# Optimization experiments

Measured on AMD Instinct MI355X. Metric: run time of the kernel, lower is better.

The kernel has to match this reference:

```python
import jax, jax.numpy as jnp
import numpy as np

N = 100_000      # nodes
E = 1_600_000    # edges
F_IN = 512       # input node features
H = 128          # hidden (num_hidden)
C = 64           # num_classes


def setup_inputs() -> dict:
    key = jax.random.key(0)
    ks = jax.random.split(key, 16)
    def lin(k, fi, fo):
        return (jax.random.normal(k, (fi, fo), jnp.float32) / np.sqrt(fi)).astype(jnp.float32)
    inp = {
        'x': jax.random.normal(ks[0], (N, F_IN), jnp.float32),
        'edge_index': jax.random.randint(ks[1], (2, E), 0, N, jnp.int32),
        'W0': lin(ks[2], F_IN, H), 'b0': jnp.zeros((H,), jnp.float32),
        'W1': lin(ks[3], H, H),    'b1': jnp.zeros((H,), jnp.float32),
        'W2': lin(ks[4], H, H),    'b2': jnp.zeros((H,), jnp.float32),
        'fc1_w': lin(ks[5], H, H), 'fc1_b': jnp.zeros((H,), jnp.float32),
        'fc2_w': lin(ks[6], H, H), 'fc2_b': jnp.zeros((H,), jnp.float32),
        'fc3_w': lin(ks[7], H, C), 'fc3_b': jnp.zeros((C,), jnp.float32),
    }
    return inp


def _gcn_norm(edge_index):
    # PyG GCNConv: add self-loops, symmetric normalization deg^-1/2 A deg^-1/2
    src = jnp.concatenate([edge_index[0], jnp.arange(N, dtype=edge_index.dtype)])
    dst = jnp.concatenate([edge_index[1], jnp.arange(N, dtype=edge_index.dtype)])
    deg = jax.ops.segment_sum(jnp.ones_like(dst, jnp.float32), dst, num_segments=N)
    dinv = jnp.where(deg > 0, jax.lax.rsqrt(deg), 0.0)
    norm = dinv[src] * dinv[dst]  # [E+N]
    return src, dst, norm


def _gcn_conv(x, W, b, src, dst, norm):
    h = x @ W + b                      # [N, H] transform first (fewer flops when F_in > H)
    msg = h[src] * norm[:, None]       # gather + scale, [E+N, H]
    return jax.ops.segment_sum(msg, dst, num_segments=N)  # scatter-add


def reference(x, edge_index, W0, b0, W1, b1, W2, b2,
              fc1_w, fc1_b, fc2_w, fc2_b, fc3_w, fc3_b):
    src, dst, norm = _gcn_norm(edge_index)
    y = jax.nn.relu(_gcn_conv(x, W0, b0, src, dst, norm))
    y = jax.nn.relu(_gcn_conv(y, W1, b1, src, dst, norm))
    y = jax.nn.relu(_gcn_conv(y, W2, b2, src, dst, norm))
    y = jax.nn.relu(y @ fc1_w + fc1_b)
    y = jax.nn.relu(y @ fc2_w + fc2_b)
    y = y @ fc3_w + fc3_b
    return jax.nn.log_softmax(y, axis=1)
```

## Files before the change

kernel.cpp:

```cpp
#include <hip/hip_runtime.h>
#include <hip/hip_bf16.h>
#include <cstdint>

typedef __hip_bfloat16 bf16;
typedef __hip_bfloat162 bf162;
typedef __bf16 bf16x8 __attribute__((ext_vector_type(8)));
typedef float f32x4 __attribute__((ext_vector_type(4)));

__global__ void detect_kernel(const unsigned short* __restrict__ xr, int* __restrict__ flag) {
  if (threadIdx.x == 0 && blockIdx.x == 0) {
    int pass = 0;
    for (int i = 0; i < 64; ++i) {
      unsigned short h = xr[2 * i];
      int e = (h >> 7) & 0xFF;
      if (e >= 110 && e <= 140) pass++;
    }
    *flag = (pass >= 32) ? 1 : 0;
  }
}

struct CvtDesc {
  const void* src;
  void* dst;
  int n, fi, fo, mode;
};
struct CvtAll { CvtDesc d[12]; };

__global__ void convert_all_kernel(CvtAll all, const int* __restrict__ flag) {
  CvtDesc dd = all.d[blockIdx.y];
  int isbf = *flag;
  for (int i = blockIdx.x * blockDim.x + threadIdx.x; i < dd.n; i += gridDim.x * blockDim.x) {
    float v = isbf ? __bfloat162float(((const bf16*)dd.src)[i]) : ((const float*)dd.src)[i];
    if (dd.mode) {
      int k = i / dd.fo, nn = i - k * dd.fo;
      ((__bf16*)dd.dst)[(size_t)nn * dd.fi + k] = (__bf16)v;
    } else {
      ((float*)dd.dst)[i] = v;
    }
  }
}


__global__ void count_kernel(const int* __restrict__ dst, int* __restrict__ deg, int E) {
  int i = blockIdx.x * blockDim.x + threadIdx.x;
  if (i < E) atomicAdd(&deg[dst[i]], 1);
}

__global__ void dinv_kernel(const int* __restrict__ deg, float* __restrict__ dinv, int n) {
  int i = blockIdx.x * blockDim.x + threadIdx.x;
  if (i < n) dinv[i] = rsqrtf((float)(deg[i] + 1));
}

__global__ void scan_block_kernel(const int* __restrict__ counts, int* __restrict__ excl,
                                  int* __restrict__ bsum, int n) {
  __shared__ int sd[1024];
  int t = threadIdx.x;
  int i = blockIdx.x * 1024 + t;
  int v = (i < n) ? counts[i] : 0;
  sd[t] = v;
  __syncthreads();
  for (int off = 1; off < 1024; off <<= 1) {
    int x = (t >= off) ? sd[t - off] : 0;
    __syncthreads();
    sd[t] += x;
    __syncthreads();
  }
  if (i < n) excl[i] = sd[t] - v;
  if (t == 1023) bsum[blockIdx.x] = sd[1023];
}

__global__ void scan_sums_kernel(int* __restrict__ bsum, int nb, int* __restrict__ row_ptr, int n) {
  __shared__ int sd[1024];
  int t = threadIdx.x;
  int v = (t < nb) ? bsum[t] : 0;
  sd[t] = v;
  __syncthreads();
  for (int off = 1; off < 1024; off <<= 1) {
    int x = (t >= off) ? sd[t - off] : 0;
    __syncthreads();
    sd[t] += x;
    __syncthreads();
  }
  if (t < nb) bsum[t] = sd[t] - v;
  if (t == 1023) row_ptr[n] = sd[1023];
}

__global__ void scan_add_kernel(int* __restrict__ excl, const int* __restrict__ bsum, int n) {
  int i = blockIdx.x * blockDim.x + threadIdx.x;
  if (i < n) excl[i] += bsum[i >> 10];
}

__global__ void fill_kernel(const int* __restrict__ src, const int* __restrict__ dst,
                            const int* __restrict__ row_ptr, int* __restrict__ cursor,
                            int* __restrict__ col, int E) {
  int i = blockIdx.x * blockDim.x + threadIdx.x;
  if (i < E) {
    int d = dst[i];
    int pos = row_ptr[d] + atomicAdd(&cursor[d], 1);
    col[pos] = src[i];
  }
}

__device__ __forceinline__ void gload_lds16(const void* g, void* l) {
  __builtin_amdgcn_global_load_lds(
      (const __attribute__((address_space(1))) void*)g,
      (__attribute__((address_space(3))) void*)l, 16, 0, 0);
}


template <int K, int ADUAL>
__global__ __launch_bounds__(256) void gemm_mfma_kernel(
    const void* __restrict__ Ain, const __bf16* __restrict__ Bt,
    const float* __restrict__ bias, bf16* __restrict__ C,
    int M, const float* __restrict__ rowscale, int do_relu,
    const int* __restrict__ flag) {
  constexpr int BK = 64;
  constexpr int NT = K / BK;
  __shared__ __align__(16) __bf16 As[2][128 * BK];
  __shared__ __align__(16) __bf16 Bs[2][128 * BK];

  const int abf = ADUAL ? flag[0] : 1;
  int t = threadIdx.x;
  int wave = t >> 6, lane = t & 63;
  int l15 = lane & 15, quad = lane >> 4;
  int wm = wave >> 1, wn = wave & 1;
  int rowbase = blockIdx.x * 128;
  const __bf16* Ab = (const __bf16*)Ain;
  const float* Af = (const float*)Ain;

  int srow = t >> 3;
  int sslot = t & 7;
  int xslot = sslot ^ (srow & 7);

  int sArow[4];
#pragma unroll
  for (int i = 0; i < 4; ++i) {
    int r = rowbase + i * 32 + srow;
    sArow[i] = (r < M) ? r : (M - 1);
  }

  f32x4 acc[4][4];
#pragma unroll
  for (int mt = 0; mt < 4; ++mt)
#pragma unroll
    for (int nt = 0; nt < 4; ++nt) acc[mt][nt] = (f32x4){0.f, 0.f, 0.f, 0.f};

  auto stage = [&](int kt, int buf) {
    int kbase = kt * BK + xslot * 8;
    if (abf) {
#pragma unroll
      for (int i = 0; i < 4; ++i)
        gload_lds16(Ab + (size_t)sArow[i] * K + kbase, &As[buf][t * 8 + i * 2048]);
    } else {
#pragma unroll
      for (int i = 0; i < 4; ++i) {
        const float* p = Af + (size_t)sArow[i] * K + kbase;
        bf16x8 v;
#pragma unroll
        for (int j = 0; j < 8; ++j) v[j] = (__bf16)p[j];
        *(bf16x8*)&As[buf][t * 8 + i * 2048] = v;
      }
    }
#pragma unroll
    for (int i = 0; i < 4; ++i)
      gload_lds16(Bt + (size_t)(i * 32 + srow) * K + kbase, &Bs[buf][t * 8 + i * 2048]);
  };

  auto compute = [&](int buf) {
#pragma unroll
    for (int c = 0; c < 2; ++c) {
      bf16x8 av[4], bv[4];
#pragma unroll
      for (int mt = 0; mt < 4; ++mt) {
        int row = wm * 64 + mt * 16 + l15;
        int slot = (c * 4 + quad) ^ (row & 7);
        av[mt] = *(const bf16x8*)&As[buf][row * BK + slot * 8];
      }
#pragma unroll
      for (int nt = 0; nt < 4; ++nt) {
        int row = wn * 64 + nt * 16 + l15;
        int slot = (c * 4 + quad) ^ (row & 7);
        bv[nt] = *(const bf16x8*)&Bs[buf][row * BK + slot * 8];
      }
#pragma unroll
      for (int mt = 0; mt < 4; ++mt)
#pragma unroll
        for (int nt = 0; nt < 4; ++nt)
          acc[mt][nt] =
              __builtin_amdgcn_mfma_f32_16x16x32_bf16(av[mt], bv[nt], acc[mt][nt], 0, 0, 0);
    }
  };

  stage(0, 0);
  __syncthreads();
#pragma unroll
  for (int kt = 0; kt < NT; ++kt) {
    int cur = kt & 1;
    if (kt + 1 < NT) stage(kt + 1, cur ^ 1);
    compute(cur);
    __syncthreads();
  }

#pragma unroll
  for (int mt = 0; mt < 4; ++mt) {
    int r0 = rowbase + wm * 64 + mt * 16 + quad * 4;
#pragma unroll
    for (int nt = 0; nt < 4; ++nt) {
      int c = wn * 64 + nt * 16 + l15;
      float bs = bias[c];
#pragma unroll
      for (int i = 0; i < 4; ++i) {
        int r = r0 + i;
        if (r < M) {
          float v = acc[mt][nt][i] + bs;
          if (rowscale) v *= rowscale[r];
          if (do_relu) v = fmaxf(v, 0.f);
          C[(size_t)r * 128 + c] = __float2bfloat16(v);
        }
      }
    }
  }
}


__global__ __launch_bounds__(256) void gather_kernel(
    const bf16* __restrict__ g, const int* __restrict__ row_ptr, const int* __restrict__ col,
    const float* __restrict__ dinv, bf16* __restrict__ y, int n) {
  int wave = threadIdx.x >> 6;
  int lane = threadIdx.x & 63;
  int node = blockIdx.x * 4 + wave;
  if (node >= n) return;
  const bf162* gp = (const bf162*)g;
  bf162 sv = gp[(size_t)node * 64 + lane];
  float ax = __bfloat162float(sv.x), ay = __bfloat162float(sv.y);
  float bx = 0.f, by = 0.f;
  int beg = row_ptr[node], end = row_ptr[node + 1];
  for (int e = beg; e < end; e += 8) {
    int s[8];
    float msk[8];
#pragma unroll
    for (int j = 0; j < 8; ++j) {
      int ee = e + j;
      bool ok = ee < end;
      s[j] = col[ok ? ee : e];
      msk[j] = ok ? 1.f : 0.f;
    }
    bf162 v[8];
#pragma unroll
    for (int j = 0; j < 8; ++j) v[j] = gp[(size_t)s[j] * 64 + lane];
#pragma unroll
    for (int j = 0; j < 8; j += 2) {
      ax = fmaf(msk[j], __bfloat162float(v[j].x), ax);
      ay = fmaf(msk[j], __bfloat162float(v[j].y), ay);
      bx = fmaf(msk[j + 1], __bfloat162float(v[j + 1].x), bx);
      by = fmaf(msk[j + 1], __bfloat162float(v[j + 1].y), by);
    }
  }
  float dv = dinv[node];
  float ox = fmaxf((ax + bx) * dv, 0.f);
  float oy = fmaxf((ay + by) * dv, 0.f);
  bf162 o;
  o.x = __float2bfloat16(ox);
  o.y = __float2bfloat16(oy);
  ((bf162*)y)[(size_t)node * 64 + lane] = o;
}


__global__ __launch_bounds__(256) void fc_chain_kernel(
    const bf16* __restrict__ yin, const __bf16* __restrict__ W1t,
    const float* __restrict__ b1, const __bf16* __restrict__ W2t,
    const float* __restrict__ b2, const __bf16* __restrict__ W3t,
    const float* __restrict__ b3, void* __restrict__ out, int M,
    const int* __restrict__ flag) {
  constexpr int LDH = 136;
  __shared__ __align__(16) __bf16 h1[128 * LDH];
  __shared__ __align__(16) __bf16 h2[128 * LDH];
  const int isbf = flag[0];
  int t = threadIdx.x;
  int wave = t >> 6, lane = t & 63;
  int l15 = lane & 15, quad = lane >> 4;
  int wm = wave >> 1, wn = wave & 1;
  int rowbase = blockIdx.x * 128;

  f32x4 acc[4][4];
  bf16x8 aA[4], bA[4], aB[4], bB[4];

  auto zacc = [&]() {
#pragma unroll
    for (int mt = 0; mt < 4; ++mt)
#pragma unroll
      for (int nt = 0; nt < 4; ++nt) acc[mt][nt] = (f32x4){0.f, 0.f, 0.f, 0.f};
  };
  auto mfma16 = [&](const bf16x8 (&av)[4], const bf16x8 (&bv)[4]) {
#pragma unroll
    for (int mt = 0; mt < 4; ++mt)
#pragma unroll
      for (int nt = 0; nt < 4; ++nt)
        acc[mt][nt] =
            __builtin_amdgcn_mfma_f32_16x16x32_bf16(av[mt], bv[nt], acc[mt][nt], 0, 0, 0);
  };

  int arow[4];
#pragma unroll
  for (int mt = 0; mt < 4; ++mt) {
    int r = rowbase + wm * 64 + mt * 16 + l15;
    arow[mt] = (r < M) ? r : (M - 1);
  }
  auto ld1 = [&](int kc, bf16x8 (&av)[4], bf16x8 (&bv)[4]) {
    int ko = kc + quad * 8;
#pragma unroll
    for (int mt = 0; mt < 4; ++mt)
      av[mt] = *(const bf16x8*)(yin + (size_t)arow[mt] * 128 + ko);
#pragma unroll
    for (int nt = 0; nt < 4; ++nt)
      bv[nt] = *(const bf16x8*)(W1t + (size_t)(wn * 64 + nt * 16 + l15) * 128 + ko);
  };
  zacc();
  ld1(0, aA, bA);
  ld1(32, aB, bB);
  mfma16(aA, bA);
  ld1(64, aA, bA);
  mfma16(aB, bB);
  ld1(96, aB, bB);
  mfma16(aA, bA);
  mfma16(aB, bB);
#pragma unroll
  for (int mt = 0; mt < 4; ++mt) {
    int rl0 = wm * 64 + mt * 16 + quad * 4;
#pragma unroll
    for (int nt = 0; nt < 4; ++nt) {
      int c = wn * 64 + nt * 16 + l15;
      float bs = b1[c];
#pragma unroll
      for (int i = 0; i < 4; ++i)
        h1[(rl0 + i) * LDH + c] = (__bf16)fmaxf(acc[mt][nt][i] + bs, 0.f);
    }
  }
  __syncthreads();

  auto ld2 = [&](int kc, bf16x8 (&av)[4], bf16x8 (&bv)[4]) {
    int ko = kc + quad * 8;
#pragma unroll
    for (int mt = 0; mt < 4; ++mt)
      av[mt] = *(const bf16x8*)&h1[(wm * 64 + mt * 16 + l15) * LDH + ko];
#pragma unroll
    for (int nt = 0; nt < 4; ++nt)
      bv[nt] = *(const bf16x8*)(W2t + (size_t)(wn * 64 + nt * 16 + l15) * 128 + ko);
  };
  zacc();
  ld2(0, aA, bA);
  ld2(32, aB, bB);
  mfma16(aA, bA);
  ld2(64, aA, bA);
  mfma16(aB, bB);
  ld2(96, aB, bB);
  mfma16(aA, bA);
  mfma16(aB, bB);
#pragma unroll
  for (int mt = 0; mt < 4; ++mt) {
    int rl0 = wm * 64 + mt * 16 + quad * 4;
#pragma unroll
    for (int nt = 0; nt < 4; ++nt) {
      int c = wn * 64 + nt * 16 + l15;
      float bs = b2[c];
#pragma unroll
      for (int i = 0; i < 4; ++i)
        h2[(rl0 + i) * LDH + c] = (__bf16)fmaxf(acc[mt][nt][i] + bs, 0.f);
    }
  }
  __syncthreads();

  f32x4 acc3[2][4];
#pragma unroll
  for (int mt = 0; mt < 2; ++mt)
#pragma unroll
    for (int nt = 0; nt < 4; ++nt) acc3[mt][nt] = (f32x4){0.f, 0.f, 0.f, 0.f};
  bf16x8 a3A[2], a3B[2];
  auto ld3 = [&](int kc, bf16x8 (&av)[2], bf16x8 (&bv)[4]) {
    int ko = kc + quad * 8;
#pragma unroll
    for (int mt = 0; mt < 2; ++mt)
      av[mt] = *(const bf16x8*)&h2[(wave * 32 + mt * 16 + l15) * LDH + ko];
#pragma unroll
    for (int nt = 0; nt < 4; ++nt)
      bv[nt] = *(const bf16x8*)(W3t + (size_t)(nt * 16 + l15) * 128 + ko);
  };
  auto mfma8 = [&](const bf16x8 (&av)[2], const bf16x8 (&bv)[4]) {
#pragma unroll
    for (int mt = 0; mt < 2; ++mt)
#pragma unroll
      for (int nt = 0; nt < 4; ++nt)
        acc3[mt][nt] =
            __builtin_amdgcn_mfma_f32_16x16x32_bf16(av[mt], bv[nt], acc3[mt][nt], 0, 0, 0);
  };
  ld3(0, a3A, bA);
  ld3(32, a3B, bB);
  mfma8(a3A, bA);
  ld3(64, a3A, bA);
  mfma8(a3B, bB);
  ld3(96, a3B, bB);
  mfma8(a3A, bA);
  mfma8(a3B, bB);

  float bcol[4];
#pragma unroll
  for (int nt = 0; nt < 4; ++nt) bcol[nt] = b3[nt * 16 + l15];

#pragma unroll
  for (int mt = 0; mt < 2; ++mt) {
#pragma unroll
    for (int i = 0; i < 4; ++i) {
      int r = rowbase + wave * 32 + mt * 16 + quad * 4 + i;
      float v0 = acc3[mt][0][i] + bcol[0];
      float v1 = acc3[mt][1][i] + bcol[1];
      float v2 = acc3[mt][2][i] + bcol[2];
      float v3 = acc3[mt][3][i] + bcol[3];
      float m = fmaxf(fmaxf(v0, v1), fmaxf(v2, v3));
#pragma unroll
      for (int off = 8; off > 0; off >>= 1) m = fmaxf(m, __shfl_xor(m, off, 16));
      float s = __expf(v0 - m) + __expf(v1 - m) + __expf(v2 - m) + __expf(v3 - m);
#pragma unroll
      for (int off = 8; off > 0; off >>= 1) s += __shfl_xor(s, off, 16);
      float ls = m + __logf(s);
      if (r < M) {
        if (isbf) {
          bf16* op = (bf16*)out + (size_t)r * 64 + l15;
          op[0] = __float2bfloat16(v0 - ls);
          op[16] = __float2bfloat16(v1 - ls);
          op[32] = __float2bfloat16(v2 - ls);
          op[48] = __float2bfloat16(v3 - ls);
        } else {
          float* op = (float*)out + (size_t)r * 64 + l15;
          op[0] = v0 - ls;
          op[16] = v1 - ls;
          op[32] = v2 - ls;
          op[48] = v3 - ls;
        }
      }
    }
  }
}


extern "C" void kernel_launch(void* const* d_in, const int* in_sizes, int n_in,
                              void* d_out, int out_size, void* d_ws, size_t ws_size,
                              hipStream_t stream) {
  const void* x = d_in[0];
  const int* ei = (const int*)d_in[1];

  const int N = in_sizes[0] / 512;
  const int E = in_sizes[1] / 2;
  const int* srcp = ei;
  const int* dstp = ei + E;

  char* ws = (char*)d_ws;
  size_t off = 0;
  auto alloc = [&](size_t bytes) {
    void* p = ws + off;
    off = (off + bytes + 255) & ~(size_t)255;
    return p;
  };
  int*    flag    = (int*)alloc(4);
  int*    deg     = (int*)alloc((size_t)N * 4);
  int*    cursor  = (int*)alloc((size_t)N * 4);
  int*    row_ptr = (int*)alloc((size_t)(N + 1) * 4);
  int*    col     = (int*)alloc((size_t)E * 4);
  float*  dinv    = (float*)alloc((size_t)N * 4);
  int*    bsum    = (int*)alloc(1024 * 4);
  __bf16* W0t     = (__bf16*)alloc((size_t)512 * 128 * 2);
  __bf16* W1t     = (__bf16*)alloc((size_t)128 * 128 * 2);
  __bf16* W2t     = (__bf16*)alloc((size_t)128 * 128 * 2);
  __bf16* fc1t    = (__bf16*)alloc((size_t)128 * 128 * 2);
  __bf16* fc2t    = (__bf16*)alloc((size_t)128 * 128 * 2);
  __bf16* fc3t    = (__bf16*)alloc((size_t)64 * 128 * 2);
  float*  b0f     = (float*)alloc(128 * 4);
  float*  b1f     = (float*)alloc(128 * 4);
  float*  b2f     = (float*)alloc(128 * 4);
  float*  fc1bf   = (float*)alloc(128 * 4);
  float*  fc2bf   = (float*)alloc(128 * 4);
  float*  fc3bf   = (float*)alloc(64 * 4);
  bf16*   gbuf    = (bf16*)alloc((size_t)N * 128 * 2);
  bf16*   ybuf    = (bf16*)alloc((size_t)N * 128 * 2);

  const int tb = 256;

  detect_kernel<<<1, 64, 0, stream>>>((const unsigned short*)x, flag);

  CvtAll ca;
  ca.d[0]  = {d_in[2],  W0t,   512 * 128, 512, 128, 1};
  ca.d[1]  = {d_in[4],  W1t,   128 * 128, 128, 128, 1};
  ca.d[2]  = {d_in[6],  W2t,   128 * 128, 128, 128, 1};
  ca.d[3]  = {d_in[8],  fc1t,  128 * 128, 128, 128, 1};
  ca.d[4]  = {d_in[10], fc2t,  128 * 128, 128, 128, 1};
  ca.d[5]  = {d_in[3],  b0f,   128, 0, 0, 0};
  ca.d[6]  = {d_in[5],  b1f,   128, 0, 0, 0};
  ca.d[7]  = {d_in[7],  b2f,   128, 0, 0, 0};
  ca.d[8]  = {d_in[9],  fc1bf, 128, 0, 0, 0};
  ca.d[9]  = {d_in[11], fc2bf, 128, 0, 0, 0};
  ca.d[10] = {d_in[12], fc3t,  128 * 64, 128, 64, 1};
  ca.d[11] = {d_in[13], fc3bf, 64, 0, 0, 0};
  convert_all_kernel<<<dim3(64, 12), 256, 0, stream>>>(ca, flag);

  hipMemsetAsync(deg, 0, (size_t)N * 4, stream);
  hipMemsetAsync(cursor, 0, (size_t)N * 4, stream);

  count_kernel<<<(E + tb - 1) / tb, tb, 0, stream>>>(dstp, deg, E);
  dinv_kernel<<<(N + tb - 1) / tb, tb, 0, stream>>>(deg, dinv, N);
  int nb = (N + 1023) / 1024;
  scan_block_kernel<<<nb, 1024, 0, stream>>>(deg, row_ptr, bsum, N);
  scan_sums_kernel<<<1, 1024, 0, stream>>>(bsum, nb, row_ptr, N);
  scan_add_kernel<<<(N + tb - 1) / tb, tb, 0, stream>>>(row_ptr, bsum, N);
  fill_kernel<<<(E + tb - 1) / tb, tb, 0, stream>>>(srcp, dstp, row_ptr, cursor, col, E);

  int gemm_blocks = (N + 127) / 128;
  int gat_blocks = (N + 3) / 4;

  gemm_mfma_kernel<512, 1><<<gemm_blocks, 256, 0, stream>>>(x, W0t, b0f, gbuf, N, dinv, 0, flag);
  gather_kernel<<<gat_blocks, 256, 0, stream>>>(gbuf, row_ptr, col, dinv, ybuf, N);
  gemm_mfma_kernel<128, 0><<<gemm_blocks, 256, 0, stream>>>(ybuf, W1t, b1f, gbuf, N, dinv, 0, flag);
  gather_kernel<<<gat_blocks, 256, 0, stream>>>(gbuf, row_ptr, col, dinv, ybuf, N);
  gemm_mfma_kernel<128, 0><<<gemm_blocks, 256, 0, stream>>>(ybuf, W2t, b2f, gbuf, N, dinv, 0, flag);
  gather_kernel<<<gat_blocks, 256, 0, stream>>>(gbuf, row_ptr, col, dinv, ybuf, N);
  fc_chain_kernel<<<gemm_blocks, 256, 0, stream>>>(ybuf, fc1t, fc1bf, fc2t, fc2bf,
                                                   fc3t, fc3bf, d_out, N, flag);
}
```

Before: 808.4 us.

## Prefetch neighbor indices in gather and add register-direct MFMA GEMM for hidden layers

The gather kernel now processes 16 neighbors per iteration and loads the next 16 column indices while the current feature rows are gathered, which hides the dependent index-load latency. A new GEMM variant for the 128-wide hidden layers loads A and B fragments straight from global memory into registers with double buffering, skipping LDS staging. The two hidden-layer GEMMs switch to it. The costs are higher register pressure, and possibly redundant global loads of B across waves that the old shared-memory path avoided.

```diff
diff --git a/kernel.cpp b/kernel.cpp
--- a/kernel.cpp
+++ b/kernel.cpp
@@ -223,6 +223,100 @@
 }
 
 
+template <int K, int ADUAL>
+__global__ __launch_bounds__(256) void gemm_mfma_reg_kernel(
+    const void* __restrict__ Ain, const __bf16* __restrict__ Bt,
+    const float* __restrict__ bias, bf16* __restrict__ C,
+    int M, const float* __restrict__ rowscale, int do_relu,
+    const int* __restrict__ flag) {
+  const int abf = ADUAL ? flag[0] : 1;
+  int t = threadIdx.x;
+  int wave = t >> 6, lane = t & 63;
+  int l15 = lane & 15, quad = lane >> 4;
+  int wm = wave >> 1, wn = wave & 1;
+  int rowbase = blockIdx.x * 128 + wm * 64;
+  int colbase = wn * 64;
+  const __bf16* Ab = (const __bf16*)Ain;
+  const float* Af = (const float*)Ain;
+
+  f32x4 acc[4][4];
+#pragma unroll
+  for (int mt = 0; mt < 4; ++mt)
+#pragma unroll
+    for (int nt = 0; nt < 4; ++nt) acc[mt][nt] = (f32x4){0.f, 0.f, 0.f, 0.f};
+
+  int arow[4];
+#pragma unroll
+  for (int mt = 0; mt < 4; ++mt) {
+    int r = rowbase + mt * 16 + l15;
+    arow[mt] = (r < M) ? r : (M - 1);
+  }
+  int brow[4];
+#pragma unroll
+  for (int nt = 0; nt < 4; ++nt) brow[nt] = colbase + nt * 16 + l15;
+
+  bf16x8 aA[4], bA[4], aB[4], bB[4];
+
+  auto load_chunk = [&](int kc, bf16x8 (&av)[4], bf16x8 (&bv)[4]) {
+    int ko = kc + quad * 8;
+    if (abf) {
+#pragma unroll
+      for (int mt = 0; mt < 4; ++mt)
+        av[mt] = *(const bf16x8*)(Ab + (size_t)arow[mt] * K + ko);
+    } else {
+#pragma unroll
+      for (int mt = 0; mt < 4; ++mt) {
+        const float* p = Af + (size_t)arow[mt] * K + ko;
+#pragma unroll
+        for (int j = 0; j < 8; ++j) av[mt][j] = (__bf16)p[j];
+      }
+    }
+#pragma unroll
+    for (int nt = 0; nt < 4; ++nt)
+      bv[nt] = *(const bf16x8*)(Bt + (size_t)brow[nt] * K + ko);
+  };
+
+  auto mfma16 = [&](const bf16x8 (&av)[4], const bf16x8 (&bv)[4]) {
+#pragma unroll
+    for (int mt = 0; mt < 4; ++mt)
+#pragma unroll
+      for (int nt = 0; nt < 4; ++nt)
+        acc[mt][nt] =
+            __builtin_amdgcn_mfma_f32_16x16x32_bf16(av[mt], bv[nt], acc[mt][nt], 0, 0, 0);
+  };
+
+  constexpr int NC = K / 32;
+  load_chunk(0, aA, bA);
+#pragma unroll
+  for (int c = 0; c < NC; c += 2) {
+    if (c + 1 < NC) load_chunk((c + 1) * 32, aB, bB);
+    mfma16(aA, bA);
+    if (c + 2 < NC) load_chunk((c + 2) * 32, aA, bA);
+    if (c + 1 < NC) mfma16(aB, bB);
+  }
+
+#pragma unroll
+  for (int mt = 0; mt < 4; ++mt) {
+    int r0 = rowbase + mt * 16 + quad * 4;
+#pragma unroll
+    for (int nt = 0; nt < 4; ++nt) {
+      int c = colbase + nt * 16 + l15;
+      float bs = bias[c];
+#pragma unroll
+      for (int i = 0; i < 4; ++i) {
+        int r = r0 + i;
+        if (r < M) {
+          float v = acc[mt][nt][i] + bs;
+          if (rowscale) v *= rowscale[r];
+          if (do_relu) v = fmaxf(v, 0.f);
+          C[(size_t)r * 128 + c] = __float2bfloat16(v);
+        }
+      }
+    }
+  }
+}
+
+
 __global__ __launch_bounds__(256) void gather_kernel(
     const bf16* __restrict__ g, const int* __restrict__ row_ptr, const int* __restrict__ col,
     const float* __restrict__ dinv, bf16* __restrict__ y, int n) {
@@ -235,25 +329,46 @@
   float ax = __bfloat162float(sv.x), ay = __bfloat162float(sv.y);
   float bx = 0.f, by = 0.f;
   int beg = row_ptr[node], end = row_ptr[node + 1];
-  for (int e = beg; e < end; e += 8) {
-    int s[8];
-    float msk[8];
-#pragma unroll
-    for (int j = 0; j < 8; ++j) {
-      int ee = e + j;
+
+  if (beg < end) {
+    int sc[16], sn[16];
+    float mc[16], mn[16];
+#pragma unroll
+    for (int j = 0; j < 16; ++j) {
+      int ee = beg + j;
       bool ok = ee < end;
-      s[j] = col[ok ? ee : e];
-      msk[j] = ok ? 1.f : 0.f;
-    }
-    bf162 v[8];
-#pragma unroll
-    for (int j = 0; j < 8; ++j) v[j] = gp[(size_t)s[j] * 64 + lane];
-#pragma unroll
-    for (int j = 0; j < 8; j += 2) {
-      ax = fmaf(msk[j], __bfloat162float(v[j].x), ax);
-      ay = fmaf(msk[j], __bfloat162float(v[j].y), ay);
-      bx = fmaf(msk[j + 1], __bfloat162float(v[j + 1].x), bx);
-      by = fmaf(msk[j + 1], __bfloat162float(v[j + 1].y), by);
+      sc[j] = col[ok ? ee : beg];
+      mc[j] = ok ? 1.f : 0.f;
+    }
+    for (int e = beg; e < end; e += 16) {
+      bf162 v[16];
+#pragma unroll
+      for (int j = 0; j < 16; ++j) v[j] = gp[(size_t)sc[j] * 64 + lane];
+      int e2 = e + 16;
+      bool more = e2 < end;
+      if (more) {
+#pragma unroll
+        for (int j = 0; j < 16; ++j) {
+          int ee = e2 + j;
+          bool ok = ee < end;
+          sn[j] = col[ok ? ee : beg];
+          mn[j] = ok ? 1.f : 0.f;
+        }
+      }
+#pragma unroll
+      for (int j = 0; j < 16; j += 2) {
+        ax = fmaf(mc[j], __bfloat162float(v[j].x), ax);
+        ay = fmaf(mc[j], __bfloat162float(v[j].y), ay);
+        bx = fmaf(mc[j + 1], __bfloat162float(v[j + 1].x), bx);
+        by = fmaf(mc[j + 1], __bfloat162float(v[j + 1].y), by);
+      }
+      if (more) {
+#pragma unroll
+        for (int j = 0; j < 16; ++j) {
+          sc[j] = sn[j];
+          mc[j] = mn[j];
+        }
+      }
     }
   }
   float dv = dinv[node];
@@ -517,9 +632,9 @@
 
   gemm_mfma_kernel<512, 1><<<gemm_blocks, 256, 0, stream>>>(x, W0t, b0f, gbuf, N, dinv, 0, flag);
   gather_kernel<<<gat_blocks, 256, 0, stream>>>(gbuf, row_ptr, col, dinv, ybuf, N);
-  gemm_mfma_kernel<128, 0><<<gemm_blocks, 256, 0, stream>>>(ybuf, W1t, b1f, gbuf, N, dinv, 0, flag);
+  gemm_mfma_reg_kernel<128, 0><<<gemm_blocks, 256, 0, stream>>>(ybuf, W1t, b1f, gbuf, N, dinv, 0, flag);
   gather_kernel<<<gat_blocks, 256, 0, stream>>>(gbuf, row_ptr, col, dinv, ybuf, N);
-  gemm_mfma_kernel<128, 0><<<gemm_blocks, 256, 0, stream>>>(ybuf, W2t, b2f, gbuf, N, dinv, 0, flag);
+  gemm_mfma_reg_kernel<128, 0><<<gemm_blocks, 256, 0, stream>>>(ybuf, W2t, b2f, gbuf, N, dinv, 0, flag);
   gather_kernel<<<gat_blocks, 256, 0, stream>>>(gbuf, row_ptr, col, dinv, ybuf, N);
   fc_chain_kernel<<<gemm_blocks, 256, 0, stream>>>(ybuf, fc1t, fc1bf, fc2t, fc2bf,
                                                    fc3t, fc3bf, d_out, N, flag);
```

After: 876.0 us. +8.4%, slower.
